# Kernel tuning notes

Measured on AMD Instinct MI355X. Metric: run time of the kernel, lower is better.

The kernel has to match this reference:

```python
import jax, jax.numpy as jnp
import numpy as np

DIM = 1024
HEADS = 16
HEAD_DIM = DIM // HEADS
HIDDEN = 4 * DIM
EPS = 1e-6


def _layer_norm(x, scale, bias):
    mu = jnp.mean(x, axis=-1, keepdims=True)
    var = jnp.mean(jnp.square(x - mu), axis=-1, keepdims=True)
    return (x - mu) * jax.lax.rsqrt(var + EPS) * scale + bias


def setup_inputs() -> dict:
    key = jax.random.key(0)
    ks = jax.random.split(key, 8)
    s = 0.02
    return {
        "x": jax.random.normal(ks[0], (8, 1024, DIM), dtype=jnp.float32),
        "w_qkv": jax.random.normal(ks[1], (DIM, 3 * DIM), dtype=jnp.float32) * s,
        "b_qkv": jnp.zeros((3 * DIM,), jnp.float32),
        "w_proj": jax.random.normal(ks[2], (DIM, DIM), dtype=jnp.float32) * s,
        "b_proj": jnp.zeros((DIM,), jnp.float32),
        "ln1_scale": jnp.ones((DIM,), jnp.float32),
        "ln1_bias": jnp.zeros((DIM,), jnp.float32),
        "ln2_scale": jnp.ones((DIM,), jnp.float32),
        "ln2_bias": jnp.zeros((DIM,), jnp.float32),
        "w_fc1": jax.random.normal(ks[3], (DIM, HIDDEN), dtype=jnp.float32) * s,
        "b_fc1": jnp.zeros((HIDDEN,), jnp.float32),
        "w_fc2": jax.random.normal(ks[4], (HIDDEN, DIM), dtype=jnp.float32) * s,
        "b_fc2": jnp.zeros((DIM,), jnp.float32),
    }


def reference(x, w_qkv, b_qkv, w_proj, b_proj, ln1_scale, ln1_bias,
              ln2_scale, ln2_bias, w_fc1, b_fc1, w_fc2, b_fc2):
    B, N, C = x.shape
    scale = HEAD_DIM ** -0.5

    # --- attention branch ---
    h = _layer_norm(x, ln1_scale, ln1_bias)
    qkv = h @ w_qkv + b_qkv                          # [B,N,3C]
    qkv = qkv.reshape(B, N, 3, HEADS, HEAD_DIM)
    qkv = jnp.transpose(qkv, (2, 0, 3, 1, 4))        # [3,B,H,N,D]
    q, k, v = qkv[0], qkv[1], qkv[2]
    attn = jnp.einsum("bhnd,bhmd->bhnm", q, k) * scale
    attn = jax.nn.softmax(attn, axis=-1)
    o = jnp.einsum("bhnm,bhmd->bhnd", attn, v)       # [B,H,N,D]
    o = jnp.transpose(o, (0, 2, 1, 3)).reshape(B, N, C)
    x = x + (o @ w_proj + b_proj)

    # --- mlp branch ---
    h = _layer_norm(x, ln2_scale, ln2_bias)
    h = jax.nn.gelu(h @ w_fc1 + b_fc1)               # tanh approx, matches flax default
    x = x + (h @ w_fc2 + b_fc2)
    return x
```

## Files before the change

### kernel.cpp

```cpp
#include <hip/hip_runtime.h>

typedef __attribute__((ext_vector_type(8))) short short8;
typedef __attribute__((ext_vector_type(4))) float f32x4;
typedef unsigned short ushort;
typedef unsigned int uint;

#define DIM 1024
#define NSEQ 1024
#define BATCH 8
#define HEADS 16
#define HD 64
#define HIDDEN 4096
#define NROWS (BATCH * NSEQ)

__device__ inline ushort f2bf(float f) {
  uint u = __float_as_uint(f);
  u += 0x7fff + ((u >> 16) & 1);
  return (ushort)(u >> 16);
}

__device__ inline f32x4 zero4() {
  f32x4 z; z[0] = 0.f; z[1] = 0.f; z[2] = 0.f; z[3] = 0.f; return z;
}

__device__ inline float gelu_fast(float x) {
  float u2 = 1.5957691216057308f * (x + 0.044715f * x * x * x);
  float e = __builtin_amdgcn_exp2f(-1.4426950408889634f * u2);
  return x / (1.0f + e);
}

#define GLDS16(g, l)                                                  \
  __builtin_amdgcn_global_load_lds(                                   \
      (const __attribute__((address_space(1))) void*)(g),             \
      (__attribute__((address_space(3))) void*)(l), 16, 0, 0)

#define WAITVM(n) asm volatile("s_waitcnt vmcnt(" #n ")" ::: "memory")
#define SBAR() asm volatile("s_barrier" ::: "memory")

__global__ __launch_bounds__(256) void ln_kernel(
    const float* __restrict__ x, const float* __restrict__ sc,
    const float* __restrict__ bi, ushort* __restrict__ out) {
  int row = blockIdx.x;
  int t = threadIdx.x;
  const float4 v = reinterpret_cast<const float4*>(x + (size_t)row * DIM)[t];
  float s = v.x + v.y + v.z + v.w;
  float s2 = v.x * v.x + v.y * v.y + v.z * v.z + v.w * v.w;
#pragma unroll
  for (int off = 32; off >= 1; off >>= 1) {
    s += __shfl_xor(s, off);
    s2 += __shfl_xor(s2, off);
  }
  __shared__ float ps[4], ps2[4];
  int w = t >> 6;
  if ((t & 63) == 0) { ps[w] = s; ps2[w] = s2; }
  __syncthreads();
  s = ps[0] + ps[1] + ps[2] + ps[3];
  s2 = ps2[0] + ps2[1] + ps2[2] + ps2[3];
  float mu = s * (1.0f / DIM);
  float var = s2 * (1.0f / DIM) - mu * mu;
  float rstd = rsqrtf(var + 1e-6f);
  float4 scv = reinterpret_cast<const float4*>(sc)[t];
  float4 biv = reinterpret_cast<const float4*>(bi)[t];
  ushort4 o;
  o.x = f2bf((v.x - mu) * rstd * scv.x + biv.x);
  o.y = f2bf((v.y - mu) * rstd * scv.y + biv.y);
  o.z = f2bf((v.z - mu) * rstd * scv.z + biv.z);
  o.w = f2bf((v.w - mu) * rstd * scv.w + biv.w);
  reinterpret_cast<ushort4*>(out + (size_t)row * DIM)[t] = o;
}

__global__ __launch_bounds__(256) void wtrans_kernel(
    const float* __restrict__ w, ushort* __restrict__ wt, int K, int N) {
  __shared__ float tile[32][33];
  int n0 = blockIdx.x * 32, k0 = blockIdx.y * 32;
  int tx = threadIdx.x & 31, ty = threadIdx.x >> 5;
#pragma unroll
  for (int j = 0; j < 4; j++)
    tile[ty + 8 * j][tx] = w[(size_t)(k0 + ty + 8 * j) * N + n0 + tx];
  __syncthreads();
#pragma unroll
  for (int j = 0; j < 4; j++)
    wt[(size_t)(n0 + ty + 8 * j) * K + k0 + tx] = f2bf(tile[tx][ty + 8 * j]);
}

__global__ __launch_bounds__(256) void vtrans_kernel(
    const ushort* __restrict__ qkv, ushort* __restrict__ vT) {
  __shared__ ushort Ts[64 * 64];
  int bh = blockIdx.y;
  int b = bh >> 4, h = bh & 15;
  int n0 = blockIdx.x * 64;
  int t = threadIdx.x;
  const ushort* src = qkv + (size_t)b * NSEQ * 3072 + 2048 + h * 64;
#pragma unroll
  for (int i = 0; i < 2; i++) {
    int ci = i * 256 + t;
    int rr = ci >> 3, c = ci & 7;
    short8 v = *reinterpret_cast<const short8*>(src + (size_t)(n0 + rr) * 3072 + c * 8);
    *reinterpret_cast<short8*>(&Ts[rr * 64 + ((c ^ (rr >> 3)) & 7) * 8]) = v;
  }
  __syncthreads();
  ushort* dst = vT + (size_t)bh * 64 * NSEQ;
#pragma unroll
  for (int i = 0; i < 2; i++) {
    int ci = i * 256 + t;
    int dd = ci >> 3, c = ci & 7;
    short8 v;
#pragma unroll
    for (int j = 0; j < 8; j++) {
      int nn = c * 8 + j;
      v[j] = (short)Ts[nn * 64 + (((dd >> 3) ^ (nn >> 3)) & 7) * 8 + (dd & 7)];
    }
    *reinterpret_cast<short8*>(dst + (size_t)dd * NSEQ + n0 + c * 8) = v;
  }
}

template <int BN, int EPI, int KK>
__global__ __launch_bounds__(512, 2) void gemm256_kernel(
    const ushort* __restrict__ A, const ushort* __restrict__ Bt,
    const float* __restrict__ bias, const float* __restrict__ res,
    void* __restrict__ outp, int M, int N) {
  constexpr int BM = 256, BK = 32;
  constexpr int WM = (BN == 256) ? 2 : 4;
  constexpr int WN = 8 / WM;
  constexpr int MR = (BM / WM) / 16;
  constexpr int NR = (BN / WN) / 16;
  constexpr int AR = 2;
  constexpr int BR = BN / 128;
  constexpr int nkt = KK / BK;
  static_assert(BN == 256 || BN == 128, "");
  static_assert(nkt >= 4 && (nkt % 2) == 0, "");

  __shared__ ushort As[4][BM * BK];
  __shared__ ushort Bs[4][BN * BK];

  int t = threadIdx.x, lane = t & 63, w = t >> 6;
  int wr = w / WN, wc = w % WN;
  int r = lane & 15, g = lane >> 4;

  int nwg = gridDim.x * gridDim.y;
  int flat = blockIdx.y * gridDim.x + blockIdx.x;
  int swzf = (flat & 7) * (nwg >> 3) + (flat >> 3);
  int bx = swzf % gridDim.x, by = swzf / gridDim.x;
  int m0 = by * BM, n0 = bx * BN;

  const ushort* Ab = A + (size_t)m0 * KK;
  const ushort* Bb = Bt + (size_t)n0 * KK;

  int srow = t >> 2;
  int sgc8 = (((t & 3) ^ (srow & 3) ^ ((srow >> 2) & 3)) & 3) * 8;
  int swb = (w << 4) * BK;
  int sw = ((g ^ (r & 3) ^ ((r >> 2) & 3)) & 3) * 8;

  auto stageAB = [&](int kt2) {
    ushort* as = &As[kt2 & 3][0];
    ushort* bs = &Bs[kt2 & 3][0];
    int ko = kt2 * BK;
#pragma unroll
    for (int p = 0; p < AR; p++)
      GLDS16(Ab + (size_t)(p * 128 + srow) * KK + ko + sgc8,
             as + p * 128 * BK + swb);
#pragma unroll
    for (int p = 0; p < BR; p++)
      GLDS16(Bb + (size_t)(p * 128 + srow) * KK + ko + sgc8,
             bs + p * 128 * BK + swb);
  };

  auto ldfrags = [&](int kt2, short8 (&fa_)[MR], short8 (&fb_)[NR]) {
    const ushort* as = &As[kt2 & 3][0];
    const ushort* bs = &Bs[kt2 & 3][0];
#pragma unroll
    for (int mi = 0; mi < MR; mi++)
      fa_[mi] = *reinterpret_cast<const short8*>(
          &as[(wr * (BM / WM) + mi * 16 + r) * BK + sw]);
#pragma unroll
    for (int ni = 0; ni < NR; ni++)
      fb_[ni] = *reinterpret_cast<const short8*>(
          &bs[(wc * (BN / WN) + ni * 16 + r) * BK + sw]);
  };

  f32x4 acc[MR][NR];
#pragma unroll
  for (int mi = 0; mi < MR; mi++)
#pragma unroll
    for (int ni = 0; ni < NR; ni++) acc[mi][ni] = zero4();

  auto body = [&](int kt, short8 (&ca)[MR], short8 (&cb)[NR],
                  short8 (&na)[MR], short8 (&nb)[NR]) {
    if (kt + 1 < nkt) ldfrags(kt + 1, na, nb);
    if (kt + 3 < nkt) stageAB(kt + 3);
    __builtin_amdgcn_s_setprio(1);
#pragma unroll
    for (int mi = 0; mi < MR; mi++)
#pragma unroll
      for (int ni = 0; ni < NR; ni++)
        acc[mi][ni] = __builtin_amdgcn_mfma_f32_16x16x32_bf16(
            ca[mi], cb[ni], acc[mi][ni], 0, 0, 0);
    __builtin_amdgcn_s_setprio(0);
    if (kt + 3 < nkt) {
      if constexpr (BN == 256) WAITVM(4); else WAITVM(3);
      SBAR();
    } else if (kt + 2 < nkt) {
      WAITVM(0);
      SBAR();
    }
  };

  stageAB(0); stageAB(1); stageAB(2);
  if constexpr (BN == 256) WAITVM(4); else WAITVM(3);
  SBAR();

  short8 fa[2][MR], fb[2][NR];
  ldfrags(0, fa[0], fb[0]);
#pragma unroll 1
  for (int k2 = 0; k2 < nkt / 2; k2++) {
    body(2 * k2 + 0, fa[0], fb[0], fa[1], fb[1]);
    body(2 * k2 + 1, fa[1], fb[1], fa[0], fb[0]);
  }

  int rg = g * 4;
#pragma unroll
  for (int mi = 0; mi < MR; mi++) {
#pragma unroll
    for (int ni = 0; ni < NR; ni++) {
      int row = m0 + wr * (BM / WM) + mi * 16 + rg;
      int col = n0 + wc * (BN / WN) + ni * 16 + r;
      float bv = bias[col];
#pragma unroll
      for (int j = 0; j < 4; j++) {
        float v = acc[mi][ni][j] + bv;
        if (EPI == 1) v = gelu_fast(v);
        if (EPI == 2) {
          reinterpret_cast<float*>(outp)[(size_t)(row + j) * N + col] =
              v + res[(size_t)(row + j) * N + col];
        } else {
          reinterpret_cast<ushort*>(outp)[(size_t)(row + j) * N + col] = f2bf(v);
        }
      }
    }
  }
}

#define SM_SCALE_L2E 0.18033688f
#define SM_BIAS_L2E 11.54156036f
__global__ __launch_bounds__(256) void attn_kernel(
    const ushort* __restrict__ qkv, const ushort* __restrict__ vT,
    ushort* __restrict__ o) {
  __shared__ ushort Kt[64 * 72];
  __shared__ ushort Vt[64 * 72];
  __shared__ ushort Pl[4][16 * 72];
  int q0 = blockIdx.x * 64, h = blockIdx.y, b = blockIdx.z;
  int t = threadIdx.x, lane = t & 63, w = t >> 6;
  int r = lane & 15, g = lane >> 4;
  const ushort* base = qkv + (size_t)b * NSEQ * 3072 + h * 64;
  const ushort* vbase = vT + (size_t)(b * HEADS + h) * 64 * NSEQ;

  short8 qf[2];
  {
    const ushort* qrow = base + (size_t)(q0 + w * 16 + r) * 3072;
    qf[0] = *reinterpret_cast<const short8*>(qrow + g * 8);
    qf[1] = *reinterpret_cast<const short8*>(qrow + 32 + g * 8);
  }

  float l[4] = {0.f, 0.f, 0.f, 0.f};
  f32x4 oacc[4];
#pragma unroll
  for (int db = 0; db < 4; db++) oacc[db] = zero4();

  int srw = t >> 3, sc8 = (t & 7) * 8;
  for (int kt = 0; kt < NSEQ / 64; kt++) {
    int k0 = kt * 64;
    short8 kreg[2], vreg[2];
#pragma unroll
    for (int i = 0; i < 2; i++) {
      int rw = srw + i * 32;
      kreg[i] = *reinterpret_cast<const short8*>(base + 1024 + (size_t)(k0 + rw) * 3072 + sc8);
      vreg[i] = *reinterpret_cast<const short8*>(vbase + (size_t)rw * NSEQ + k0 + sc8);
    }
    __syncthreads();
#pragma unroll
    for (int i = 0; i < 2; i++) {
      int rw = srw + i * 32;
      *reinterpret_cast<short8*>(&Kt[rw * 72 + sc8]) = kreg[i];
      *reinterpret_cast<short8*>(&Vt[rw * 72 + sc8]) = vreg[i];
    }
    __syncthreads();

#pragma unroll
    for (int kb = 0; kb < 4; kb++) {
      short8 kf0 = *reinterpret_cast<const short8*>(&Kt[(kb * 16 + r) * 72 + g * 8]);
      short8 kf1 = *reinterpret_cast<const short8*>(&Kt[(kb * 16 + r) * 72 + 32 + g * 8]);
      f32x4 z = zero4();
      z = __builtin_amdgcn_mfma_f32_16x16x32_bf16(qf[0], kf0, z, 0, 0, 0);
      z = __builtin_amdgcn_mfma_f32_16x16x32_bf16(qf[1], kf1, z, 0, 0, 0);
#pragma unroll
      for (int j = 0; j < 4; j++) {
        float p = __builtin_amdgcn_exp2f(fmaf(z[j], SM_SCALE_L2E, -SM_BIAS_L2E));
        l[j] += p;
        Pl[w][(g * 4 + j) * 72 + kb * 16 + r] = (ushort)(__float_as_uint(p) >> 16);
      }
    }

#pragma unroll
    for (int ks = 0; ks < 2; ks++) {
      short8 pa = *reinterpret_cast<const short8*>(&Pl[w][r * 72 + ks * 32 + g * 8]);
#pragma unroll
      for (int db = 0; db < 4; db++) {
        short8 vb = *reinterpret_cast<const short8*>(&Vt[(db * 16 + r) * 72 + ks * 32 + g * 8]);
        oacc[db] = __builtin_amdgcn_mfma_f32_16x16x32_bf16(pa, vb, oacc[db], 0, 0, 0);
      }
    }
  }

#pragma unroll
  for (int j = 0; j < 4; j++) {
#pragma unroll
    for (int off = 8; off >= 1; off >>= 1) l[j] += __shfl_xor(l[j], off);
    l[j] = 1.0f / l[j];
  }

#pragma unroll
  for (int db = 0; db < 4; db++)
#pragma unroll
    for (int j = 0; j < 4; j++) {
      size_t row = (size_t)b * NSEQ + q0 + w * 16 + g * 4 + j;
      int col = h * 64 + db * 16 + r;
      o[row * DIM + col] = f2bf(oacc[db][j] * l[j]);
    }
}

extern "C" void kernel_launch(void* const* d_in, const int* in_sizes, int n_in,
                              void* d_out, int out_size, void* d_ws, size_t ws_size,
                              hipStream_t stream) {
  const float* x      = (const float*)d_in[0];
  const float* w_qkv  = (const float*)d_in[1];
  const float* b_qkv  = (const float*)d_in[2];
  const float* w_proj = (const float*)d_in[3];
  const float* b_proj = (const float*)d_in[4];
  const float* ln1s   = (const float*)d_in[5];
  const float* ln1b   = (const float*)d_in[6];
  const float* ln2s   = (const float*)d_in[7];
  const float* ln2b   = (const float*)d_in[8];
  const float* w_fc1  = (const float*)d_in[9];
  const float* b_fc1  = (const float*)d_in[10];
  const float* w_fc2  = (const float*)d_in[11];
  const float* b_fc2  = (const float*)d_in[12];
  float* out = (float*)d_out;

  char* ws = (char*)d_ws;
  ushort* wqkv_t  = (ushort*)(ws);
  ushort* wproj_t = (ushort*)(ws + 6291456);
  ushort* wfc1_t  = (ushort*)(ws + 8388608);
  ushort* wfc2_t  = (ushort*)(ws + 16777216);
  ushort* hbuf    = (ushort*)(ws + 25165824);
  float*  x1      = (float*)(ws + 41943040);
  ushort* vTb     = (ushort*)(ws + 41943040);
  ushort* qkv     = (ushort*)(ws + 75497472);
  ushort* obuf    = (ushort*)(ws + 125829120);
  ushort* fc1a    = qkv;

  wtrans_kernel<<<dim3(3072 / 32, 1024 / 32), 256, 0, stream>>>(w_qkv, wqkv_t, 1024, 3072);
  wtrans_kernel<<<dim3(1024 / 32, 1024 / 32), 256, 0, stream>>>(w_proj, wproj_t, 1024, 1024);
  wtrans_kernel<<<dim3(4096 / 32, 1024 / 32), 256, 0, stream>>>(w_fc1, wfc1_t, 1024, 4096);
  wtrans_kernel<<<dim3(1024 / 32, 4096 / 32), 256, 0, stream>>>(w_fc2, wfc2_t, 4096, 1024);

  ln_kernel<<<NROWS, 256, 0, stream>>>(x, ln1s, ln1b, hbuf);
  gemm256_kernel<128, 0, 1024><<<dim3(3072 / 128, NROWS / 256), 512, 0, stream>>>(
      hbuf, wqkv_t, b_qkv, nullptr, qkv, NROWS, 3072);
  vtrans_kernel<<<dim3(NSEQ / 64, BATCH * HEADS), 256, 0, stream>>>(qkv, vTb);
  attn_kernel<<<dim3(NSEQ / 64, HEADS, BATCH), 256, 0, stream>>>(qkv, vTb, obuf);
  gemm256_kernel<128, 2, 1024><<<dim3(1024 / 128, NROWS / 256), 512, 0, stream>>>(
      obuf, wproj_t, b_proj, x, x1, NROWS, 1024);

  ln_kernel<<<NROWS, 256, 0, stream>>>(x1, ln2s, ln2b, hbuf);
  gemm256_kernel<256, 1, 1024><<<dim3(4096 / 256, NROWS / 256), 512, 0, stream>>>(
      hbuf, wfc1_t, b_fc1, nullptr, fc1a, NROWS, 4096);
  gemm256_kernel<128, 2, 4096><<<dim3(1024 / 128, NROWS / 256), 512, 0, stream>>>(
      fc1a, wfc2_t, b_fc2, x1, out, NROWS, 1024);
}
```

Baseline: 389.7 us.

## Use a 128x128-tile GEMM kernel with grid swizzle for the FC1 layer

```diff
diff --git a/kernel.cpp b/kernel.cpp
--- a/kernel.cpp
+++ b/kernel.cpp
@@ -240,6 +240,102 @@
   }
 }
 
+template <int EPI>
+__global__ __launch_bounds__(256, 3) void gemm128_kernel(
+    const ushort* __restrict__ A, const ushort* __restrict__ Bt,
+    const float* __restrict__ bias, const float* __restrict__ res,
+    void* __restrict__ outp, int M, int N, int K) {
+  constexpr int BM = 128, BN = 128, BK = 32;
+
+  __shared__ ushort As[2][BM * BK];
+  __shared__ ushort Bs[2][BN * BK];
+
+  int t = threadIdx.x, lane = t & 63, w = t >> 6;
+  int wr = w >> 1, wc = w & 1;
+  int r = lane & 15, g = lane >> 4;
+
+  int nwg = gridDim.x * gridDim.y;
+  int flat = blockIdx.y * gridDim.x + blockIdx.x;
+  int swzf = (flat & 7) * (nwg >> 3) + (flat >> 3);
+  int bx = swzf % gridDim.x, by = swzf / gridDim.x;
+  int m0 = by * BM, n0 = bx * BN;
+
+  const ushort* Ab = A + (size_t)m0 * K;
+  const ushort* Bb = Bt + (size_t)n0 * K;
+
+  int srow = t >> 2;
+  int sgc8 = (((t & 3) ^ (srow & 3) ^ ((srow >> 2) & 3)) & 3) * 8;
+  int swb = (t >> 6) * 16 * BK;
+  int sw = ((g ^ (r & 3) ^ ((r >> 2) & 3)) & 3) * 8;
+
+  f32x4 acc[4][4];
+#pragma unroll
+  for (int mi = 0; mi < 4; mi++)
+#pragma unroll
+    for (int ni = 0; ni < 4; ni++) acc[mi][ni] = zero4();
+
+  int nkt = K / BK;
+#pragma unroll
+  for (int p = 0; p < 2; p++) {
+    GLDS16(Ab + (size_t)(p * 64 + srow) * K + sgc8, &As[0][(p * 64) * BK + swb]);
+    GLDS16(Bb + (size_t)(p * 64 + srow) * K + sgc8, &Bs[0][(p * 64) * BK + swb]);
+  }
+  __syncthreads();
+
+  int cur = 0;
+  for (int kt = 0; kt < nkt; kt++) {
+    if (kt + 1 < nkt) {
+      int ko = (kt + 1) * BK;
+#pragma unroll
+      for (int p = 0; p < 2; p++) {
+        GLDS16(Ab + (size_t)(p * 64 + srow) * K + ko + sgc8,
+               &As[cur ^ 1][(p * 64) * BK + swb]);
+        GLDS16(Bb + (size_t)(p * 64 + srow) * K + ko + sgc8,
+               &Bs[cur ^ 1][(p * 64) * BK + swb]);
+      }
+    }
+    short8 a[4], b[4];
+#pragma unroll
+    for (int mi = 0; mi < 4; mi++)
+      a[mi] = *reinterpret_cast<const short8*>(
+          &As[cur][(wr * 64 + mi * 16 + r) * BK + sw]);
+#pragma unroll
+    for (int ni = 0; ni < 4; ni++)
+      b[ni] = *reinterpret_cast<const short8*>(
+          &Bs[cur][(wc * 64 + ni * 16 + r) * BK + sw]);
+#pragma unroll
+    for (int mi = 0; mi < 4; mi++)
+#pragma unroll
+      for (int ni = 0; ni < 4; ni++)
+        acc[mi][ni] = __builtin_amdgcn_mfma_f32_16x16x32_bf16(
+            a[mi], b[ni], acc[mi][ni], 0, 0, 0);
+    __syncthreads();
+    cur ^= 1;
+  }
+
+  int rg = g * 4;
+#pragma unroll
+  for (int mi = 0; mi < 4; mi++) {
+#pragma unroll
+    for (int ni = 0; ni < 4; ni++) {
+      int row = m0 + wr * 64 + mi * 16 + rg;
+      int col = n0 + wc * 64 + ni * 16 + r;
+      float bv = bias[col];
+#pragma unroll
+      for (int j = 0; j < 4; j++) {
+        float v = acc[mi][ni][j] + bv;
+        if (EPI == 1) v = gelu_fast(v);
+        if (EPI == 2) {
+          reinterpret_cast<float*>(outp)[(size_t)(row + j) * N + col] =
+              v + res[(size_t)(row + j) * N + col];
+        } else {
+          reinterpret_cast<ushort*>(outp)[(size_t)(row + j) * N + col] = f2bf(v);
+        }
+      }
+    }
+  }
+}
+
 #define SM_SCALE_L2E 0.18033688f
 #define SM_BIAS_L2E 11.54156036f
 __global__ __launch_bounds__(256) void attn_kernel(
@@ -372,8 +468,8 @@
       obuf, wproj_t, b_proj, x, x1, NROWS, 1024);
 
   ln_kernel<<<NROWS, 256, 0, stream>>>(x1, ln2s, ln2b, hbuf);
-  gemm256_kernel<256, 1, 1024><<<dim3(4096 / 256, NROWS / 256), 512, 0, stream>>>(
-      hbuf, wfc1_t, b_fc1, nullptr, fc1a, NROWS, 4096);
+  gemm128_kernel<1><<<dim3(4096 / 128, NROWS / 128), 256, 0, stream>>>(
+      hbuf, wfc1_t, b_fc1, nullptr, fc1a, NROWS, 4096, 1024);
   gemm256_kernel<128, 2, 4096><<<dim3(1024 / 128, NROWS / 256), 512, 0, stream>>>(
       fc1a, wfc2_t, b_fc2, x1, out, NROWS, 1024);
 }
```

Measured after the change: 397.8 us. 1.02x slower.
